# Kernel tuning notes

Hardware: AMD Instinct MI355X
Metric: run time of the kernel (lower is better)

The kernel has to match this reference:

```python
import math
import jax, jax.numpy as jnp
import numpy as np

B, S, G, D = 16, 256, 2048, 512
H = 8
DK = D // H  # per-head key dim
E = 8        # num experts
TOPK = 2


def setup_inputs() -> dict:
    key = jax.random.key(0)
    ks = jax.random.split(key, 12)
    init = lambda k, shape, fan_in: jax.random.uniform(k, shape, jnp.float32, -1.0, 1.0) / np.sqrt(fan_in)
    return {
        'query': jax.random.normal(ks[0], (B, S, D), jnp.float32),
        'key': jax.random.normal(ks[1], (B, G, D), jnp.float32),
        'value': jax.random.normal(ks[2], (B, G, D), jnp.float32),  # unused by module (MHA uses h=key)
        'logit_key': jax.random.normal(ks[3], (B, G, D), jnp.float32),
        'attn_mask': jnp.zeros((B, G), dtype=bool),
        'Wq': init(ks[4], (H, D, DK), D),
        'Wk': init(ks[5], (H, D, DK), D),
        'Wv': init(ks[6], (H, D, DK), D),
        'Wo': init(ks[7], (H, DK, D), DK),
        'w_gate': jnp.zeros((D, E), jnp.float32) + init(ks[8], (D, E), D) * 0.0 + init(ks[9], (D, E), D),
        'expert_w': init(ks[10], (E, D, D), D),
    }


def _mha_glimpse(query, h, attn_mask, Wq, Wk, Wv, Wo):
    # Kool-style MHA: K and V both derived from h
    Q = jnp.einsum('bsd,hdk->bhsk', query, Wq)
    K = jnp.einsum('bgd,hdk->bhgk', h, Wk)
    V = jnp.einsum('bgd,hdk->bhgk', h, Wv)
    scores = jnp.einsum('bhsk,bhgk->bhsg', Q, K) / math.sqrt(DK)
    # 2D mask (B,G) expanded over heads and steps; True = masked out
    mask = attn_mask[:, None, None, :]
    scores = jnp.where(mask, jnp.float32(-1e9), scores)
    attn = jax.nn.softmax(scores, axis=-1)
    heads = jnp.einsum('bhsg,bhgk->bhsk', attn, V)
    return jnp.einsum('bhsk,hkd->bsd', heads, Wo)


def _moe(x, w_gate, expert_w):
    # x: (N, D). Noisy top-k gating, eval mode (no noise): clean logits -> top-k -> softmax over top-k.
    logits = x @ w_gate                                  # (N, E)
    top_vals, top_idx = jax.lax.top_k(logits, TOPK)      # (N, k)
    top_gates = jax.nn.softmax(top_vals, axis=-1)        # (N, k)
    gates = jnp.sum(jax.nn.one_hot(top_idx, E, dtype=x.dtype) * top_gates[..., None], axis=1)  # (N, E)
    expert_out = jnp.einsum('nd,edo->neo', x, expert_w)  # dense combine: same math as dispatch/scatter
    return jnp.einsum('ne,neo->no', gates, expert_out)


def reference(query, key, value, logit_key, attn_mask, Wq, Wk, Wv, Wo, w_gate, expert_w):
    glimpse = _mha_glimpse(query, key, attn_mask, Wq, Wk, Wv, Wo)  # (B, S, D)
    gm = _moe(glimpse.reshape(B * S, D), w_gate, expert_w).reshape(B, S, D)
    logits = jnp.einsum('bsd,bgd->bsg', gm, logit_key) / math.sqrt(D)
    return logits
```

## Files before the change

kernel.cpp:

```cpp
#include <hip/hip_runtime.h>

#define B_  16
#define S_  256
#define G_  2048
#define D_  512
#define H_  8
#define DK_ 64
#define E_  8

typedef _Float16 half8  __attribute__((ext_vector_type(8)));
typedef _Float16 half4v __attribute__((ext_vector_type(4)));
typedef float    floatx4 __attribute__((ext_vector_type(4)));

#define GLDS(g, l) __builtin_amdgcn_global_load_lds( \
    (const __attribute__((address_space(1))) void*)(g), \
    (__attribute__((address_space(3))) void*)(l), 16, 0, 0)

__global__ void __launch_bounds__(256) split_f16(
    const float* __restrict__ src, _Float16* __restrict__ hi,
    _Float16* __restrict__ lo, int n4)
{
    int i = blockIdx.x * 256 + threadIdx.x;
    if (i >= n4) return;
    float4 v = ((const float4*)src)[i];
    half4v h, l;
    h[0] = (_Float16)v.x; h[1] = (_Float16)v.y;
    h[2] = (_Float16)v.z; h[3] = (_Float16)v.w;
    l[0] = (_Float16)(v.x - (float)h[0]); l[1] = (_Float16)(v.y - (float)h[1]);
    l[2] = (_Float16)(v.z - (float)h[2]); l[3] = (_Float16)(v.w - (float)h[3]);
    ((half4v*)hi)[i] = h;
    ((half4v*)lo)[i] = l;
}

__global__ void __launch_bounds__(256) transpose_split(
    const float* __restrict__ src, _Float16* __restrict__ hi,
    _Float16* __restrict__ lo, int R, int C)
{
    __shared__ float T[32][33];
    const int tid = threadIdx.x;
    const long zo = (long)blockIdx.z * R * C;
    const int r0 = blockIdx.y * 32, c0 = blockIdx.x * 32;
#pragma unroll
    for (int p = 0; p < 4; ++p) {
        int i = tid + p * 256;
        int lr = i >> 5, lc = i & 31;
        T[lr][lc] = src[zo + (long)(r0 + lr) * C + (c0 + lc)];
    }
    __syncthreads();
#pragma unroll
    for (int p = 0; p < 4; ++p) {
        int i = tid + p * 256;
        int orr = i >> 5, oc = i & 31;
        float v = T[oc][orr];
        _Float16 h = (_Float16)v;
        long o = zo + (long)(c0 + orr) * R + (r0 + oc);
        hi[o] = h;
        lo[o] = (_Float16)(v - (float)h);
    }
}

__global__ void __launch_bounds__(256) gemm_f16x3(
    const _Float16* __restrict__ Ah, const _Float16* __restrict__ Al,
    const _Float16* __restrict__ Bh, const _Float16* __restrict__ Bl,
    float* __restrict__ C, _Float16* __restrict__ Chi, _Float16* __restrict__ Clo,
    long ldc, long sAz, long sBz, long sCz, float alpha)
{
    __shared__ _Float16 Ash[128 * 32], Asl[128 * 32];
    __shared__ _Float16 Bsh[128 * 32], Bsl[128 * 32];
    const int tid = threadIdx.x;
    const int w = tid >> 6, lane = tid & 63;
    const int quad = lane >> 4, tn = lane & 15;
    const int wm = (w >> 1) * 64, wn = (w & 1) * 64;
    const int z = blockIdx.z;
    const long m0 = (long)blockIdx.y * 128;
    const long n0 = (long)blockIdx.x * 128;
    const _Float16* Agh = Ah + (z * sAz + m0) * 512;
    const _Float16* Agl = Al + (z * sAz + m0) * 512;
    const _Float16* Bgh = Bh + (z * sBz + n0) * 512;
    const _Float16* Bgl = Bl + (z * sBz + n0) * 512;
    const long glane = (long)(lane >> 2) * 512 + (lane & 3) * 8;

    floatx4 acc[4][4] = {};

    for (int k0 = 0; k0 < 512; k0 += 32) {
#pragma unroll
        for (int cc = 0; cc < 2; ++cc) {
            const int c = 2 * w + cc;
            const long go = (long)c * 16 * 512 + glane + k0;
            GLDS(Agh + go, Ash + c * 512);
            GLDS(Agl + go, Asl + c * 512);
            GLDS(Bgh + go, Bsh + c * 512);
            GLDS(Bgl + go, Bsl + c * 512);
        }
        asm volatile("s_waitcnt vmcnt(0)" ::: "memory");
        __syncthreads();

        half8 ah[4], al[4], bh[4], bl[4];
#pragma unroll
        for (int t = 0; t < 4; ++t) {
            ah[t] = *(const half8*)&Ash[(wm + t * 16 + tn) * 32 + quad * 8];
            al[t] = *(const half8*)&Asl[(wm + t * 16 + tn) * 32 + quad * 8];
            bh[t] = *(const half8*)&Bsh[(wn + t * 16 + tn) * 32 + quad * 8];
            bl[t] = *(const half8*)&Bsl[(wn + t * 16 + tn) * 32 + quad * 8];
        }
#pragma unroll
        for (int i = 0; i < 4; ++i)
#pragma unroll
            for (int j = 0; j < 4; ++j) {
                acc[i][j] = __builtin_amdgcn_mfma_f32_16x16x32_f16(ah[i], bh[j], acc[i][j], 0, 0, 0);
                acc[i][j] = __builtin_amdgcn_mfma_f32_16x16x32_f16(ah[i], bl[j], acc[i][j], 0, 0, 0);
                acc[i][j] = __builtin_amdgcn_mfma_f32_16x16x32_f16(al[i], bh[j], acc[i][j], 0, 0, 0);
            }
        __syncthreads();
    }

#pragma unroll
    for (int i = 0; i < 4; ++i) {
        const long row0 = m0 + wm + i * 16 + quad * 4;
#pragma unroll
        for (int r = 0; r < 4; ++r) {
            const long row = row0 + r;
#pragma unroll
            for (int j = 0; j < 4; ++j) {
                float v = acc[i][j][r] * alpha;
                const long o = (long)z * sCz + row * ldc + n0 + wn + j * 16 + tn;
                if (C) C[o] = v;
                if (Chi) {
                    _Float16 hh = (_Float16)v;
                    Chi[o] = hh;
                    Clo[o] = (_Float16)(v - (float)hh);
                }
            }
        }
    }
}

__global__ void __launch_bounds__(512) flash_mfma(
    const _Float16* __restrict__ qh, const _Float16* __restrict__ qlo,
    const _Float16* __restrict__ kh, const _Float16* __restrict__ kl,
    const _Float16* __restrict__ vh, const _Float16* __restrict__ vl,
    const unsigned char* __restrict__ mask,
    float* __restrict__ Opart, float* __restrict__ Lpart)
{
    __shared__ half8 KH[512], KL[512], VH[512], VL[512];
    __shared__ float PLb[8 * 16 * 64];
    const int tid = threadIdx.x;
    const int wid = tid >> 6, lane = tid & 63;
    const int quad = lane >> 4, tn = lane & 15;
    const int h = blockIdx.y, b = blockIdx.z;
    const int sblk = blockIdx.x & 1, gh = blockIdx.x >> 1;
    const int gbase0 = gh * 1024;
    const int s_base = sblk * 128 + wid * 16;
    const long tok0 = (long)b * S_ + s_base;
    float* Pw = PLb + wid * (16 * 64);
    const unsigned char* mb = mask + (long)b * G_;

    const long qoff = (tok0 + tn) * 512 + h * 64 + quad * 8;
    half8 qfh[2], qfl[2];
    qfh[0] = *(const half8*)(qh + qoff);
    qfh[1] = *(const half8*)(qh + qoff + 32);
    qfl[0] = *(const half8*)(qlo + qoff);
    qfl[1] = *(const half8*)(qlo + qoff + 32);

    const int sr = tid >> 3, sg = tid & 7;
    const int swz = sr * 8 + (sg ^ (sr & 7));
    const long kgbase = (long)b * G_ * 512 + h * 64 + sg * 8;
    const long vgbase = (long)(h * 64 + sr) * (B_ * G_) + (long)b * G_ + sg * 8;

    half8 pk0 = *(const half8*)(kh + kgbase + (long)(gbase0 + sr) * 512);
    half8 pk1 = *(const half8*)(kl + kgbase + (long)(gbase0 + sr) * 512);
    half8 pk2 = *(const half8*)(vh + vgbase + gbase0);
    half8 pk3 = *(const half8*)(vl + vgbase + gbase0);

    floatx4 accO[4] = {};
    float lsum[4] = {0.f, 0.f, 0.f, 0.f};

    for (int t = 0; t < 16; ++t) {
        KH[swz] = pk0; KL[swz] = pk1; VH[swz] = pk2; VL[swz] = pk3;
        __syncthreads();
        if (t < 15) {
            const int g1 = gbase0 + (t + 1) * 64;
            pk0 = *(const half8*)(kh + kgbase + (long)(g1 + sr) * 512);
            pk1 = *(const half8*)(kl + kgbase + (long)(g1 + sr) * 512);
            pk2 = *(const half8*)(vh + vgbase + g1);
            pk3 = *(const half8*)(vl + vgbase + g1);
        }
        const int g0 = gbase0 + t * 64;

        floatx4 accS[4] = {};
#pragma unroll
        for (int k0 = 0; k0 < 2; ++k0)
#pragma unroll
            for (int nj = 0; nj < 4; ++nj) {
                const int row = nj * 16 + tn;
                const int gi = row * 8 + ((k0 * 4 + quad) ^ (row & 7));
                half8 kbh = KH[gi], kbl = KL[gi];
                accS[nj] = __builtin_amdgcn_mfma_f32_16x16x32_f16(qfh[k0], kbh, accS[nj], 0, 0, 0);
                accS[nj] = __builtin_amdgcn_mfma_f32_16x16x32_f16(qfh[k0], kbl, accS[nj], 0, 0, 0);
                accS[nj] = __builtin_amdgcn_mfma_f32_16x16x32_f16(qfl[k0], kbh, accS[nj], 0, 0, 0);
            }

        float rs[4] = {0.f, 0.f, 0.f, 0.f};
#pragma unroll
        for (int nj = 0; nj < 4; ++nj) {
            const bool mk = mb[g0 + nj * 16 + tn] != 0;
#pragma unroll
            for (int rr = 0; rr < 4; ++rr) {
                float p = __builtin_exp2f(accS[nj][rr]);
                p = mk ? 0.0f : p;
                accS[nj][rr] = p;
                rs[rr] += p;
            }
        }
#pragma unroll
        for (int rr = 0; rr < 4; ++rr) {
            float v = rs[rr];
            v += __shfl_xor(v, 1); v += __shfl_xor(v, 2);
            v += __shfl_xor(v, 4); v += __shfl_xor(v, 8);
            lsum[rr] += v;
        }

#pragma unroll
        for (int nj = 0; nj < 4; ++nj)
#pragma unroll
            for (int rr = 0; rr < 4; ++rr) {
                const int srow = quad * 4 + rr;
                const int c = nj * 16 + tn;
                Pw[srow * 64 + ((((c >> 2) ^ srow) & 15) << 2) + (c & 3)] = accS[nj][rr];
            }
        asm volatile("s_waitcnt lgkmcnt(0)" ::: "memory");

#pragma unroll
        for (int k0 = 0; k0 < 2; ++k0) {
            const int ga = k0 * 8 + quad * 2;
            floatx4 p0 = *(floatx4*)&Pw[tn * 64 + (((ga ^ tn) & 15) << 2)];
            floatx4 p1 = *(floatx4*)&Pw[tn * 64 + ((((ga + 1) ^ tn) & 15) << 2)];
            half8 ph, pl;
#pragma unroll
            for (int e = 0; e < 8; ++e) {
                const float x = (e < 4) ? p0[e & 3] : p1[e & 3];
                const float hi = __uint_as_float(__float_as_uint(x) & 0xFFFFE000u);
                ph[e] = (_Float16)hi;
                pl[e] = (_Float16)(x - hi);
            }
#pragma unroll
            for (int nj = 0; nj < 4; ++nj) {
                const int row = nj * 16 + tn;
                const int gi = row * 8 + ((k0 * 4 + quad) ^ (row & 7));
                half8 vbh = VH[gi], vbl = VL[gi];
                accO[nj] = __builtin_amdgcn_mfma_f32_16x16x32_f16(ph, vbh, accO[nj], 0, 0, 0);
                accO[nj] = __builtin_amdgcn_mfma_f32_16x16x32_f16(ph, vbl, accO[nj], 0, 0, 0);
                accO[nj] = __builtin_amdgcn_mfma_f32_16x16x32_f16(pl, vbh, accO[nj], 0, 0, 0);
            }
        }
        __syncthreads();
    }

    float* Op = Opart + (long)gh * (4096L * 512);
#pragma unroll
    for (int rr = 0; rr < 4; ++rr) {
        const long rbase = (tok0 + quad * 4 + rr) * 512 + h * 64 + tn;
#pragma unroll
        for (int nj = 0; nj < 4; ++nj)
            Op[rbase + nj * 16] = accO[nj][rr];
    }
    if (tn == 0) {
#pragma unroll
        for (int rr = 0; rr < 4; ++rr)
            Lpart[(long)gh * 32768 + (tok0 + quad * 4 + rr) * 8 + h] = lsum[rr];
    }
}

__global__ void __launch_bounds__(256) combine_flash(
    const float* __restrict__ Op, const float* __restrict__ Lp,
    _Float16* __restrict__ hd_hi, _Float16* __restrict__ hd_lo)
{
    const int idx = blockIdx.x * 256 + threadIdx.x;
    const int n = idx >> 7;
    const int c = (idx & 127) * 4;
    const int h = c >> 6;
    const float l = Lp[(long)n * 8 + h] + Lp[32768 + (long)n * 8 + h];
    const float inv = 1.0f / l;
    float4 a = *(const float4*)(Op + (long)n * 512 + c);
    float4 d = *(const float4*)(Op + 2097152L + (long)n * 512 + c);
    const float ox = (a.x + d.x) * inv;
    const float oy = (a.y + d.y) * inv;
    const float oz = (a.z + d.z) * inv;
    const float ow = (a.w + d.w) * inv;
    half4v hh, ll;
    hh[0] = (_Float16)ox; hh[1] = (_Float16)oy;
    hh[2] = (_Float16)oz; hh[3] = (_Float16)ow;
    ll[0] = (_Float16)(ox - (float)hh[0]); ll[1] = (_Float16)(oy - (float)hh[1]);
    ll[2] = (_Float16)(oz - (float)hh[2]); ll[3] = (_Float16)(ow - (float)hh[3]);
    *(half4v*)(hd_hi + (long)n * 512 + c) = hh;
    *(half4v*)(hd_lo + (long)n * 512 + c) = ll;
}

__global__ void __launch_bounds__(256) gate_topk(
    const _Float16* __restrict__ Xh, const _Float16* __restrict__ Xl,
    const float* __restrict__ wg, float* __restrict__ gates)
{
    __shared__ float W[512][8];
    __shared__ float Xs[256][37];
    const int tid = threadIdx.x;
    const int n0 = blockIdx.x * 256;
#pragma unroll
    for (int p = 0; p < 16; ++p) ((float*)W)[tid + p * 256] = wg[tid + p * 256];

    float acc[8] = {};
    for (int dc = 0; dc < 512; dc += 32) {
        __syncthreads();
#pragma unroll
        for (int p = 0; p < 8; ++p) {
            int f = tid + p * 256;
            int row = f >> 3, c4 = f & 7;
            long o = (long)(n0 + row) * 512 + dc + 4 * c4;
            half4v hv = *(const half4v*)(Xh + o);
            half4v lv = *(const half4v*)(Xl + o);
#pragma unroll
            for (int i = 0; i < 4; ++i) Xs[row][4 * c4 + i] = (float)hv[i] + (float)lv[i];
        }
        __syncthreads();
        for (int d2 = 0; d2 < 32; ++d2) {
            float xv = Xs[tid][d2];
#pragma unroll
            for (int e = 0; e < 8; ++e) acc[e] += xv * W[dc + d2][e];
        }
    }
    float v1 = -3.0e38f; int i1 = 0;
#pragma unroll
    for (int e = 0; e < 8; ++e) if (acc[e] > v1) { v1 = acc[e]; i1 = e; }
    float v2 = -3.0e38f; int i2 = -1;
#pragma unroll
    for (int e = 0; e < 8; ++e) if (e != i1 && acc[e] > v2) { v2 = acc[e]; i2 = e; }
    float t = __expf(v2 - v1);
    float g1 = 1.0f / (1.0f + t);
    float g2 = t / (1.0f + t);
#pragma unroll
    for (int e = 0; e < 8; ++e)
        gates[(long)(n0 + tid) * 8 + e] = (e == i1) ? g1 : ((e == i2) ? g2 : 0.0f);
}

__global__ void __launch_bounds__(256) combine_moe(
    const float* __restrict__ eo, const float* __restrict__ gates,
    _Float16* __restrict__ gh, _Float16* __restrict__ gl)
{
    const int idx = blockIdx.x * 256 + threadIdx.x;
    const int n = idx >> 7;
    const int c = (idx & 127) * 4;
    float g[8];
#pragma unroll
    for (int e = 0; e < 8; ++e) g[e] = gates[(long)n * 8 + e];
    float ax = 0.f, ay = 0.f, az = 0.f, aw = 0.f;
#pragma unroll
    for (int e = 0; e < 8; ++e) {
        if (g[e] != 0.0f) {
            float4 v = *(const float4*)(eo + (long)e * 2097152 + (long)n * 512 + c);
            ax += g[e] * v.x; ay += g[e] * v.y; az += g[e] * v.z; aw += g[e] * v.w;
        }
    }
    half4v h, l;
    h[0] = (_Float16)ax; h[1] = (_Float16)ay; h[2] = (_Float16)az; h[3] = (_Float16)aw;
    l[0] = (_Float16)(ax - (float)h[0]); l[1] = (_Float16)(ay - (float)h[1]);
    l[2] = (_Float16)(az - (float)h[2]); l[3] = (_Float16)(aw - (float)h[3]);
    *(half4v*)(gh + (long)n * 512 + c) = h;
    *(half4v*)(gl + (long)n * 512 + c) = l;
}

extern "C" void kernel_launch(void* const* d_in, const int* in_sizes, int n_in,
                              void* d_out, int out_size, void* d_ws, size_t ws_size,
                              hipStream_t stream) {
    const float* query     = (const float*)d_in[0];
    const float* key       = (const float*)d_in[1];
    const float* logit_key = (const float*)d_in[3];
    const unsigned char* mask = (const unsigned char*)d_in[4];
    const float* Wq = (const float*)d_in[5];
    const float* Wk = (const float*)d_in[6];
    const float* Wv = (const float*)d_in[7];
    const float* Wo = (const float*)d_in[8];
    const float* wg = (const float*)d_in[9];
    const float* Ew = (const float*)d_in[10];
    float* out = (float*)d_out;

    const size_t MBy = 1048576;
    char* W = (char*)d_ws;
    _Float16* q_hi  = (_Float16*)(W + 0 * MBy);
    _Float16* q_lo  = (_Float16*)(W + 4 * MBy);
    _Float16* kp_hi = (_Float16*)(W + 8 * MBy);
    _Float16* kp_lo = (_Float16*)(W + 40 * MBy);
    _Float16* vt_hi = (_Float16*)(W + 72 * MBy);
    _Float16* vt_lo = (_Float16*)(W + 104 * MBy);
    _Float16* kin_hi = (_Float16*)(W + 136 * MBy);
    _Float16* kin_lo = (_Float16*)(W + 168 * MBy);
    float*    Opart = (float*)(W + 136 * MBy);
    float*    Lpart = (float*)(W + 153 * MBy);
    float*    eo    = (float*)(W + 136 * MBy);
    _Float16* lk_hi = (_Float16*)(W + 136 * MBy);
    _Float16* lk_lo = (_Float16*)(W + 168 * MBy);
    _Float16* wq_hi = (_Float16*)(W + 204 * MBy);
    _Float16* wq_lo = (_Float16*)(W + 204 * MBy + 524288);
    _Float16* wk_hi = (_Float16*)(W + 205 * MBy);
    _Float16* wk_lo = (_Float16*)(W + 205 * MBy + 524288);
    _Float16* wv_hi = (_Float16*)(W + 206 * MBy);
    _Float16* wv_lo = (_Float16*)(W + 206 * MBy + 524288);
    _Float16* wo_hi = (_Float16*)(W + 207 * MBy);
    _Float16* wo_lo = (_Float16*)(W + 207 * MBy + 524288);
    _Float16* ew_hi = (_Float16*)(W + 208 * MBy);
    _Float16* ew_lo = (_Float16*)(W + 212 * MBy);
    _Float16* qi_hi = (_Float16*)(W + 216 * MBy);
    _Float16* qi_lo = (_Float16*)(W + 220 * MBy);
    _Float16* hd_hi = (_Float16*)(W + 216 * MBy);
    _Float16* hd_lo = (_Float16*)(W + 220 * MBy);
    _Float16* gl_hi = (_Float16*)(W + 224 * MBy);
    _Float16* gl_lo = (_Float16*)(W + 228 * MBy);
    _Float16* gm_hi = (_Float16*)(W + 232 * MBy);
    _Float16* gm_lo = (_Float16*)(W + 236 * MBy);
    float*    gates = (float*)(W + 240 * MBy);

    dim3 blk(256);

    split_f16<<<dim3(16384), blk, 0, stream>>>(key, kin_hi, kin_lo, 4194304);
    split_f16<<<dim3(2048), blk, 0, stream>>>(query, qi_hi, qi_lo, 524288);
    transpose_split<<<dim3(2, 16, 8), blk, 0, stream>>>(Wq, wq_hi, wq_lo, 512, 64);
    transpose_split<<<dim3(2, 16, 8), blk, 0, stream>>>(Wk, wk_hi, wk_lo, 512, 64);
    transpose_split<<<dim3(2, 16, 8), blk, 0, stream>>>(Wv, wv_hi, wv_lo, 512, 64);
    transpose_split<<<dim3(16, 16, 1), blk, 0, stream>>>(Wo, wo_hi, wo_lo, 512, 512);
    transpose_split<<<dim3(16, 16, 8), blk, 0, stream>>>(Ew, ew_hi, ew_lo, 512, 512);

    gemm_f16x3<<<dim3(4, 32, 1), blk, 0, stream>>>(
        qi_hi, qi_lo, wq_hi, wq_lo, nullptr, q_hi, q_lo, 512, 0, 0, 0,
        0.1803368801111204f);
    gemm_f16x3<<<dim3(4, 256, 1), blk, 0, stream>>>(
        kin_hi, kin_lo, wk_hi, wk_lo, nullptr, kp_hi, kp_lo, 512, 0, 0, 0, 1.0f);
    gemm_f16x3<<<dim3(256, 4, 1), blk, 0, stream>>>(
        wv_hi, wv_lo, kin_hi, kin_lo, nullptr, vt_hi, vt_lo, (long)B_ * G_,
        0, 0, 0, 1.0f);

    flash_mfma<<<dim3(4, H_, B_), dim3(512), 0, stream>>>(
        q_hi, q_lo, kp_hi, kp_lo, vt_hi, vt_lo, mask, Opart, Lpart);
    combine_flash<<<dim3(2048), blk, 0, stream>>>(Opart, Lpart, hd_hi, hd_lo);

    gemm_f16x3<<<dim3(4, 32, 1), blk, 0, stream>>>(
        hd_hi, hd_lo, wo_hi, wo_lo, nullptr, gl_hi, gl_lo, 512, 0, 0, 0, 1.0f);

    gate_topk<<<dim3(16), blk, 0, stream>>>(gl_hi, gl_lo, wg, gates);

    gemm_f16x3<<<dim3(4, 32, 8), blk, 0, stream>>>(
        gl_hi, gl_lo, ew_hi, ew_lo, eo, nullptr, nullptr, 512, 0, 512, 2097152, 1.0f);

    combine_moe<<<dim3(2048), blk, 0, stream>>>(eo, gates, gm_hi, gm_lo);

    split_f16<<<dim3(16384), blk, 0, stream>>>(logit_key, lk_hi, lk_lo, 4194304);

    gemm_f16x3<<<dim3(16, 2, 16), blk, 0, stream>>>(
        gm_hi, gm_lo, lk_hi, lk_lo, out, nullptr, nullptr, 2048,
        256, 2048, 524288, 0.04419417382415922f);
}
```

Before: 627.1 us.

## Rewrite flash attention with 32x32 MFMA, direct-to-LDS loads, and 4-way G split

Rewrites the attention kernel to use 32x32x16 MFMA tiles and 256-thread blocks, with each wave covering 32 query rows. The G dimension is split four ways instead of two, so the grid doubles. K and V tiles now load straight into LDS with global_load_lds instead of being staged through registers. P is exchanged across lanes with shuffles instead of an LDS round trip, and the mask is precomputed into a 64-bit bitmap so fully unmasked tiles skip the mask step. The combine kernel now reduces four partials, which adds partial-buffer traffic, and loads are no longer prefetched one tile ahead.

```diff
diff --git a/kernel.cpp b/kernel.cpp
--- a/kernel.cpp
+++ b/kernel.cpp
@@ -11,6 +11,7 @@
 typedef _Float16 half8  __attribute__((ext_vector_type(8)));
 typedef _Float16 half4v __attribute__((ext_vector_type(4)));
 typedef float    floatx4 __attribute__((ext_vector_type(4)));
+typedef float    floatx16 __attribute__((ext_vector_type(16)));
 
 #define GLDS(g, l) __builtin_amdgcn_global_load_lds( \
     (const __attribute__((address_space(1))) void*)(g), \
@@ -57,6 +58,19 @@
         hi[o] = h;
         lo[o] = (_Float16)(v - (float)h);
     }
+}
+
+__global__ void __launch_bounds__(512) mask_bitmap(
+    const unsigned char* __restrict__ mask, unsigned long long* __restrict__ bmp)
+{
+    const int t = threadIdx.x;
+    const int b = t >> 5, tile = t & 31;
+    const unsigned char* m = mask + (long)b * G_ + tile * 64;
+    unsigned long long v = 0ULL;
+#pragma unroll
+    for (int i = 0; i < 64; ++i)
+        v |= (unsigned long long)(m[i] ? 1u : 0u) << i;
+    bmp[t] = v;
 }
 
 __global__ void __launch_bounds__(256) gemm_f16x3(
@@ -135,140 +149,140 @@
     }
 }
 
-__global__ void __launch_bounds__(512) flash_mfma(
+__global__ void __launch_bounds__(256) flash_mfma(
     const _Float16* __restrict__ qh, const _Float16* __restrict__ qlo,
     const _Float16* __restrict__ kh, const _Float16* __restrict__ kl,
     const _Float16* __restrict__ vh, const _Float16* __restrict__ vl,
-    const unsigned char* __restrict__ mask,
+    const unsigned long long* __restrict__ bmp,
     float* __restrict__ Opart, float* __restrict__ Lpart)
 {
     __shared__ half8 KH[512], KL[512], VH[512], VL[512];
-    __shared__ float PLb[8 * 16 * 64];
     const int tid = threadIdx.x;
     const int wid = tid >> 6, lane = tid & 63;
-    const int quad = lane >> 4, tn = lane & 15;
-    const int h = blockIdx.y, b = blockIdx.z;
-    const int sblk = blockIdx.x & 1, gh = blockIdx.x >> 1;
-    const int gbase0 = gh * 1024;
-    const int s_base = sblk * 128 + wid * 16;
-    const long tok0 = (long)b * S_ + s_base;
-    float* Pw = PLb + wid * (16 * 64);
-    const unsigned char* mb = mask + (long)b * G_;
-
-    const long qoff = (tok0 + tn) * 512 + h * 64 + quad * 8;
-    half8 qfh[2], qfl[2];
-    qfh[0] = *(const half8*)(qh + qoff);
-    qfh[1] = *(const half8*)(qh + qoff + 32);
-    qfl[0] = *(const half8*)(qlo + qoff);
-    qfl[1] = *(const half8*)(qlo + qoff + 32);
-
-    const int sr = tid >> 3, sg = tid & 7;
-    const int swz = sr * 8 + (sg ^ (sr & 7));
-    const long kgbase = (long)b * G_ * 512 + h * 64 + sg * 8;
-    const long vgbase = (long)(h * 64 + sr) * (B_ * G_) + (long)b * G_ + sg * 8;
-
-    half8 pk0 = *(const half8*)(kh + kgbase + (long)(gbase0 + sr) * 512);
-    half8 pk1 = *(const half8*)(kl + kgbase + (long)(gbase0 + sr) * 512);
-    half8 pk2 = *(const half8*)(vh + vgbase + gbase0);
-    half8 pk3 = *(const half8*)(vl + vgbase + gbase0);
-
-    floatx4 accO[4] = {};
-    float lsum[4] = {0.f, 0.f, 0.f, 0.f};
-
-    for (int t = 0; t < 16; ++t) {
-        KH[swz] = pk0; KL[swz] = pk1; VH[swz] = pk2; VL[swz] = pk3;
-        __syncthreads();
-        if (t < 15) {
-            const int g1 = gbase0 + (t + 1) * 64;
-            pk0 = *(const half8*)(kh + kgbase + (long)(g1 + sr) * 512);
-            pk1 = *(const half8*)(kl + kgbase + (long)(g1 + sr) * 512);
-            pk2 = *(const half8*)(vh + vgbase + g1);
-            pk3 = *(const half8*)(vl + vgbase + g1);
-        }
-        const int g0 = gbase0 + t * 64;
-
-        floatx4 accS[4] = {};
-#pragma unroll
-        for (int k0 = 0; k0 < 2; ++k0)
-#pragma unroll
-            for (int nj = 0; nj < 4; ++nj) {
-                const int row = nj * 16 + tn;
-                const int gi = row * 8 + ((k0 * 4 + quad) ^ (row & 7));
+    const int lh = lane >> 5, ln = lane & 31;
+    const int head = blockIdx.y, b = blockIdx.z;
+    const int sblk = blockIdx.x & 1, gq = blockIdx.x >> 1;
+    const long tok0 = (long)b * S_ + sblk * 128 + wid * 32;
+
+    const long qoff = (tok0 + ln) * 512 + head * 64 + lh * 8;
+    half8 qfh[4], qfl[4];
+#pragma unroll
+    for (int ks = 0; ks < 4; ++ks) {
+        qfh[ks] = *(const half8*)(qh + qoff + ks * 16);
+        qfl[ks] = *(const half8*)(qlo + qoff + ks * 16);
+    }
+
+    const int srow_lo = lane >> 3;
+    const int sgs = lane & 7;
+    const long kgK = (long)b * G_ * 512 + head * 64;
+    const long kgV = (long)head * 64 * (B_ * G_) + (long)b * G_;
+
+    floatx16 accO[2] = {};
+    float lsum = 0.f;
+
+    for (int t = 0; t < 8; ++t) {
+        const int g0 = gq * 512 + t * 64;
+#pragma unroll
+        for (int cc = 0; cc < 2; ++cc) {
+            const int c = 2 * wid + cc;
+            const int r = c * 8 + srow_lo;
+            const int gs = sgs ^ (r & 7);
+            const long ko = kgK + (long)(g0 + r) * 512 + gs * 8;
+            const long vo = kgV + (long)r * (B_ * G_) + g0 + gs * 8;
+            GLDS(kh + ko, KH + c * 64);
+            GLDS(kl + ko, KL + c * 64);
+            GLDS(vh + vo, VH + c * 64);
+            GLDS(vl + vo, VL + c * 64);
+        }
+        asm volatile("s_waitcnt vmcnt(0)" ::: "memory");
+        __syncthreads();
+
+        floatx16 accS[2] = {};
+#pragma unroll
+        for (int gt = 0; gt < 2; ++gt) {
+            const int grow = gt * 32 + ln;
+            const int gbase = grow * 8, gswz = grow & 7;
+#pragma unroll
+            for (int ks = 0; ks < 4; ++ks) {
+                const int gi = gbase + ((ks * 2 + lh) ^ gswz);
                 half8 kbh = KH[gi], kbl = KL[gi];
-                accS[nj] = __builtin_amdgcn_mfma_f32_16x16x32_f16(qfh[k0], kbh, accS[nj], 0, 0, 0);
-                accS[nj] = __builtin_amdgcn_mfma_f32_16x16x32_f16(qfh[k0], kbl, accS[nj], 0, 0, 0);
-                accS[nj] = __builtin_amdgcn_mfma_f32_16x16x32_f16(qfl[k0], kbh, accS[nj], 0, 0, 0);
-            }
-
-        float rs[4] = {0.f, 0.f, 0.f, 0.f};
-#pragma unroll
-        for (int nj = 0; nj < 4; ++nj) {
-            const bool mk = mb[g0 + nj * 16 + tn] != 0;
-#pragma unroll
-            for (int rr = 0; rr < 4; ++rr) {
-                float p = __builtin_exp2f(accS[nj][rr]);
-                p = mk ? 0.0f : p;
-                accS[nj][rr] = p;
-                rs[rr] += p;
-            }
-        }
-#pragma unroll
-        for (int rr = 0; rr < 4; ++rr) {
-            float v = rs[rr];
-            v += __shfl_xor(v, 1); v += __shfl_xor(v, 2);
-            v += __shfl_xor(v, 4); v += __shfl_xor(v, 8);
-            lsum[rr] += v;
-        }
-
-#pragma unroll
-        for (int nj = 0; nj < 4; ++nj)
-#pragma unroll
-            for (int rr = 0; rr < 4; ++rr) {
-                const int srow = quad * 4 + rr;
-                const int c = nj * 16 + tn;
-                Pw[srow * 64 + ((((c >> 2) ^ srow) & 15) << 2) + (c & 3)] = accS[nj][rr];
-            }
-        asm volatile("s_waitcnt lgkmcnt(0)" ::: "memory");
-
-#pragma unroll
-        for (int k0 = 0; k0 < 2; ++k0) {
-            const int ga = k0 * 8 + quad * 2;
-            floatx4 p0 = *(floatx4*)&Pw[tn * 64 + (((ga ^ tn) & 15) << 2)];
-            floatx4 p1 = *(floatx4*)&Pw[tn * 64 + ((((ga + 1) ^ tn) & 15) << 2)];
-            half8 ph, pl;
-#pragma unroll
-            for (int e = 0; e < 8; ++e) {
-                const float x = (e < 4) ? p0[e & 3] : p1[e & 3];
-                const float hi = __uint_as_float(__float_as_uint(x) & 0xFFFFE000u);
-                ph[e] = (_Float16)hi;
-                pl[e] = (_Float16)(x - hi);
-            }
-#pragma unroll
-            for (int nj = 0; nj < 4; ++nj) {
-                const int row = nj * 16 + tn;
-                const int gi = row * 8 + ((k0 * 4 + quad) ^ (row & 7));
-                half8 vbh = VH[gi], vbl = VL[gi];
-                accO[nj] = __builtin_amdgcn_mfma_f32_16x16x32_f16(ph, vbh, accO[nj], 0, 0, 0);
-                accO[nj] = __builtin_amdgcn_mfma_f32_16x16x32_f16(ph, vbl, accO[nj], 0, 0, 0);
-                accO[nj] = __builtin_amdgcn_mfma_f32_16x16x32_f16(pl, vbh, accO[nj], 0, 0, 0);
-            }
-        }
-        __syncthreads();
-    }
-
-    float* Op = Opart + (long)gh * (4096L * 512);
-#pragma unroll
-    for (int rr = 0; rr < 4; ++rr) {
-        const long rbase = (tok0 + quad * 4 + rr) * 512 + h * 64 + tn;
-#pragma unroll
-        for (int nj = 0; nj < 4; ++nj)
-            Op[rbase + nj * 16] = accO[nj][rr];
-    }
-    if (tn == 0) {
-#pragma unroll
-        for (int rr = 0; rr < 4; ++rr)
-            Lpart[(long)gh * 32768 + (tok0 + quad * 4 + rr) * 8 + h] = lsum[rr];
-    }
+                accS[gt] = __builtin_amdgcn_mfma_f32_32x32x16_f16(kbh, qfh[ks], accS[gt], 0, 0, 0);
+                accS[gt] = __builtin_amdgcn_mfma_f32_32x32x16_f16(kbh, qfl[ks], accS[gt], 0, 0, 0);
+                accS[gt] = __builtin_amdgcn_mfma_f32_32x32x16_f16(kbl, qfh[ks], accS[gt], 0, 0, 0);
+            }
+        }
+
+        const unsigned long long bm = bmp[(b << 5) + (g0 >> 6)];
+        if (bm != 0ULL) {
+            const unsigned w0 = lh ? ((unsigned)bm >> 4) : (unsigned)bm;
+            const unsigned w1 = lh ? ((unsigned)(bm >> 32) >> 4) : (unsigned)(bm >> 32);
+#pragma unroll
+            for (int gt = 0; gt < 2; ++gt) {
+                const unsigned wsel = gt ? w1 : w0;
+#pragma unroll
+                for (int r = 0; r < 16; ++r) {
+                    const int sh = (r & 3) + 8 * (r >> 2);
+                    if ((wsel >> sh) & 1u) accS[gt][r] = -1.0e9f;
+                }
+            }
+        }
+
+        float rs = 0.f;
+#pragma unroll
+        for (int gt = 0; gt < 2; ++gt)
+#pragma unroll
+            for (int r = 0; r < 16; ++r) {
+                const float pv = __builtin_exp2f(accS[gt][r]);
+                accS[gt][r] = pv;
+                rs += pv;
+            }
+        rs += __shfl_xor(rs, 32);
+        lsum += rs;
+
+#pragma unroll
+        for (int gt = 0; gt < 2; ++gt)
+#pragma unroll
+            for (int w = 0; w < 2; ++w) {
+                half8 ph, pl;
+#pragma unroll
+                for (int j = 0; j < 4; ++j) {
+                    const float pA = accS[gt][8 * w + j];
+                    const float pB = accS[gt][8 * w + 4 + j];
+                    const float snd = lh ? pA : pB;
+                    const float rcv = __shfl_xor(snd, 32);
+                    const float e03 = lh ? rcv : pA;
+                    const float e47 = lh ? pB : rcv;
+                    float hi = __uint_as_float(__float_as_uint(e03) & 0xFFFFE000u);
+                    ph[j] = (_Float16)hi;
+                    pl[j] = (_Float16)(e03 - hi);
+                    hi = __uint_as_float(__float_as_uint(e47) & 0xFFFFE000u);
+                    ph[4 + j] = (_Float16)hi;
+                    pl[4 + j] = (_Float16)(e47 - hi);
+                }
+                const int gvb = gt * 4 + w * 2 + lh;
+#pragma unroll
+                for (int nt = 0; nt < 2; ++nt) {
+                    const int vrow = nt * 32 + ln;
+                    const int gi = vrow * 8 + (gvb ^ (vrow & 7));
+                    half8 vbh = VH[gi], vbl = VL[gi];
+                    accO[nt] = __builtin_amdgcn_mfma_f32_32x32x16_f16(ph, vbh, accO[nt], 0, 0, 0);
+                    accO[nt] = __builtin_amdgcn_mfma_f32_32x32x16_f16(ph, vbl, accO[nt], 0, 0, 0);
+                    accO[nt] = __builtin_amdgcn_mfma_f32_32x32x16_f16(pl, vbh, accO[nt], 0, 0, 0);
+                }
+            }
+        __syncthreads();
+    }
+
+    float* Op = Opart + (long)gq * (4096L * 512);
+#pragma unroll
+    for (int nt = 0; nt < 2; ++nt)
+#pragma unroll
+        for (int r = 0; r < 16; ++r) {
+            const int s = (r & 3) + 8 * (r >> 2) + 4 * lh;
+            Op[(tok0 + s) * 512 + head * 64 + nt * 32 + ln] = accO[nt][r];
+        }
+    if (lane < 32)
+        Lpart[(long)gq * 32768 + (tok0 + lane) * 8 + head] = lsum;
 }
 
 __global__ void __launch_bounds__(256) combine_flash(
@@ -279,14 +293,17 @@
     const int n = idx >> 7;
     const int c = (idx & 127) * 4;
     const int h = c >> 6;
-    const float l = Lp[(long)n * 8 + h] + Lp[32768 + (long)n * 8 + h];
+    float l = 0.f;
+#pragma unroll
+    for (int q = 0; q < 4; ++q) l += Lp[q * 32768 + (long)n * 8 + h];
     const float inv = 1.0f / l;
     float4 a = *(const float4*)(Op + (long)n * 512 + c);
-    float4 d = *(const float4*)(Op + 2097152L + (long)n * 512 + c);
-    const float ox = (a.x + d.x) * inv;
-    const float oy = (a.y + d.y) * inv;
-    const float oz = (a.z + d.z) * inv;
-    const float ow = (a.w + d.w) * inv;
+#pragma unroll
+    for (int q = 1; q < 4; ++q) {
+        float4 d = *(const float4*)(Op + (long)q * 2097152 + (long)n * 512 + c);
+        a.x += d.x; a.y += d.y; a.z += d.z; a.w += d.w;
+    }
+    const float ox = a.x * inv, oy = a.y * inv, oz = a.z * inv, ow = a.w * inv;
     half4v hh, ll;
     hh[0] = (_Float16)ox; hh[1] = (_Float16)oy;
     hh[2] = (_Float16)oz; hh[3] = (_Float16)ow;
@@ -393,7 +410,7 @@
     _Float16* kin_hi = (_Float16*)(W + 136 * MBy);
     _Float16* kin_lo = (_Float16*)(W + 168 * MBy);
     float*    Opart = (float*)(W + 136 * MBy);
-    float*    Lpart = (float*)(W + 153 * MBy);
+    float*    Lpart = (float*)(W + 168 * MBy);
     float*    eo    = (float*)(W + 136 * MBy);
     _Float16* lk_hi = (_Float16*)(W + 136 * MBy);
     _Float16* lk_lo = (_Float16*)(W + 168 * MBy);
@@ -416,11 +433,13 @@
     _Float16* gm_hi = (_Float16*)(W + 232 * MBy);
     _Float16* gm_lo = (_Float16*)(W + 236 * MBy);
     float*    gates = (float*)(W + 240 * MBy);
+    unsigned long long* bmp = (unsigned long long*)(W + 240 * MBy + 131072);
 
     dim3 blk(256);
 
     split_f16<<<dim3(16384), blk, 0, stream>>>(key, kin_hi, kin_lo, 4194304);
     split_f16<<<dim3(2048), blk, 0, stream>>>(query, qi_hi, qi_lo, 524288);
+    mask_bitmap<<<dim3(1), dim3(512), 0, stream>>>(mask, bmp);
     transpose_split<<<dim3(2, 16, 8), blk, 0, stream>>>(Wq, wq_hi, wq_lo, 512, 64);
     transpose_split<<<dim3(2, 16, 8), blk, 0, stream>>>(Wk, wk_hi, wk_lo, 512, 64);
     transpose_split<<<dim3(2, 16, 8), blk, 0, stream>>>(Wv, wv_hi, wv_lo, 512, 64);
@@ -436,8 +455,8 @@
         wv_hi, wv_lo, kin_hi, kin_lo, nullptr, vt_hi, vt_lo, (long)B_ * G_,
         0, 0, 0, 1.0f);
 
-    flash_mfma<<<dim3(4, H_, B_), dim3(512), 0, stream>>>(
-        q_hi, q_lo, kp_hi, kp_lo, vt_hi, vt_lo, mask, Opart, Lpart);
+    flash_mfma<<<dim3(8, H_, B_), blk, 0, stream>>>(
+        q_hi, q_lo, kp_hi, kp_lo, vt_hi, vt_lo, bmp, Opart, Lpart);
     combine_flash<<<dim3(2048), blk, 0, stream>>>(Opart, Lpart, hd_hi, hd_lo);
 
     gemm_f16x3<<<dim3(4, 32, 1), blk, 0, stream>>>(
```

Measured after the change: 617.6 us. About the same (-1.5%).
